# Optimization experiments

Measured on AMD Instinct MI355X. Metric: run time of the kernel, lower is better.

## Reference

```python
import jax, jax.numpy as jnp
from jax import lax
import numpy as np
import math

B, L, UNITS, DM, P = 2048, 2, 16, 512, 16
CH = UNITS // P            # 1  (attention 'head' dim c)
D = DM // P                # 32
C_ATT = CH * D             # 32 channels in patch space
C_FFN = 4 * C_ATT          # 128
HALF = P // 2              # 8 (post-stride-2 patch size)
EPS = 1e-5


def _to_patches(x):
    # 'b (c p1) (d p2) -> b (c d) p1 p2'
    b = x.shape[0]
    x = x.reshape(b, CH, P, D, P).transpose(0, 1, 3, 2, 4)
    return x.reshape(b, CH * D, P, P)


def _from_patches(x):
    # 'b (c d) p1 p2 -> b (c p1) (d p2)'
    b = x.shape[0]
    x = x.reshape(b, CH, D, P, P).transpose(0, 1, 3, 2, 4)
    return x.reshape(b, CH * P, D * P)


def _layernorm(x, g, b):
    m = jnp.mean(x, -1, keepdims=True)
    v = jnp.mean((x - m) ** 2, -1, keepdims=True)
    return (x - m) * lax.rsqrt(v + EPS) * g + b


def _dw_block(x, dw_w, dw_b, bn_g, bn_b, bn_m, bn_v, pw_w, pw_b, stride):
    # depthwise 3x3 conv -> BatchNorm (eval) -> 1x1 pointwise conv
    C = x.shape[1]
    y = lax.conv_general_dilated(
        x, dw_w[:, None], (stride, stride), [(1, 1), (1, 1)],
        dimension_numbers=('NCHW', 'OIHW', 'NCHW'), feature_group_count=C)
    if dw_b is not None:
        y = y + dw_b[None, :, None, None]
    scale = (bn_g * lax.rsqrt(bn_v + EPS))[None, :, None, None]
    y = (y - bn_m[None, :, None, None]) * scale + bn_b[None, :, None, None]
    y = jnp.einsum('bchw,oc->bohw', y, pw_w)
    if pw_b is not None:
        y = y + pw_b[None, :, None, None]
    return y


def _encoder(x, ln1_g, ln1_b, ln2_g, ln2_b, qkv_dw, qkv_bng, qkv_bnb, qkv_bnm,
             qkv_bnv, qkv_pw, position, c1d_w, c1d_b, lin_w, lin_b,
             f1_w, f1_b, fdw_w, fdw_b, f_bng, f_bnb, f_bnm, f_bnv,
             fpw_w, fpw_b, f2_w, f2_b):
    b = x.shape[0]
    for l in range(L):
        # ---- attention sublayer (pre-norm) ----
        x1 = _layernorm(x, ln1_g[l], ln1_b[l])
        xp = _to_patches(x1)                              # (B, 32, 16, 16)
        qkv = [_dw_block(xp, qkv_dw[l, i], None,
                         qkv_bng[l, i], qkv_bnb[l, i], qkv_bnm[l, i], qkv_bnv[l, i],
                         qkv_pw[l, i], None, 2)           # (B, 32, 8, 8)
               .reshape(b, CH, D, HALF * HALF)            # 'b (c d) p1 p2 -> b c d (p1 p2)'
               for i in range(3)]
        q, k, v = qkv
        scores = jnp.einsum('bcde,bcfe->bcdf', q, k) / math.sqrt(HALF * HALF)
        scores = scores + position[l][None]               # (B, 1, 32, 32)
        p_attn = jax.nn.softmax(scores, axis=-1)
        o = jnp.einsum('bcdf,bcfe->bcde', p_attn, v)      # (B, 1, 32, 64)
        # 'b c d (p1 p2) -> b (c p1) (d p2)' with p1 = P//2
        o = o.reshape(b, CH, D, HALF, HALF).transpose(0, 1, 3, 2, 4)
        o = o.reshape(b, CH * HALF, D * HALF)             # (B, 8, 256)
        o = jnp.einsum('bcd,oc->bod', o, c1d_w[l]) + c1d_b[l][None, :, None]
        o = jnp.einsum('bcd,od->bco', o, lin_w[l]) + lin_b[l]  # (B, 16, 512)
        x = x + o
        # ---- conv-FFN sublayer ----
        x2 = _layernorm(x, ln2_g[l], ln2_b[l])
        y = _to_patches(x2)                               # (B, 32, 16, 16)
        y = jnp.einsum('bchw,oc->bohw', y, f1_w[l]) + f1_b[l][None, :, None, None]
        y = jax.nn.relu(y)                                # (B, 128, 16, 16)
        y = _dw_block(y, fdw_w[l], fdw_b[l], f_bng[l], f_bnb[l], f_bnm[l],
                      f_bnv[l], fpw_w[l], fpw_b[l], 1)
        y = jax.nn.relu(y)
        y = jnp.einsum('bchw,oc->bohw', y, f2_w[l]) + f2_b[l][None, :, None, None]
        x = x + _from_patches(y)
    return x


def setup_inputs():
    key = jax.random.key(0)
    ks = iter(jax.random.split(key, 16))
    nrm = lambda shape, s=0.05: jax.random.normal(next(ks), shape, jnp.float32) * s
    return dict(
        x=jax.random.normal(next(ks), (B, UNITS, DM), jnp.float32),
        ln1_g=jnp.ones((L, DM)), ln1_b=jnp.zeros((L, DM)),
        ln2_g=jnp.ones((L, DM)), ln2_b=jnp.zeros((L, DM)),
        qkv_dw=nrm((L, 3, C_ATT, 3, 3)),
        qkv_bng=jnp.ones((L, 3, C_ATT)), qkv_bnb=jnp.zeros((L, 3, C_ATT)),
        qkv_bnm=jnp.zeros((L, 3, C_ATT)), qkv_bnv=jnp.ones((L, 3, C_ATT)),
        qkv_pw=nrm((L, 3, C_ATT, C_ATT)),
        position=nrm((L, CH, D, D), 1.0),
        c1d_w=nrm((L, UNITS, UNITS // 2)), c1d_b=jnp.zeros((L, UNITS)),
        lin_w=nrm((L, DM, DM // 2)), lin_b=jnp.zeros((L, DM)),
        f1_w=nrm((L, C_FFN, C_ATT)), f1_b=jnp.zeros((L, C_FFN)),
        fdw_w=nrm((L, C_FFN, 3, 3)), fdw_b=jnp.zeros((L, C_FFN)),
        f_bng=jnp.ones((L, C_FFN)), f_bnb=jnp.zeros((L, C_FFN)),
        f_bnm=jnp.zeros((L, C_FFN)), f_bnv=jnp.ones((L, C_FFN)),
        fpw_w=nrm((L, C_FFN, C_FFN)), fpw_b=jnp.zeros((L, C_FFN)),
        f2_w=nrm((L, C_ATT, C_FFN)), f2_b=jnp.zeros((L, C_ATT)),
    )


def reference(x, ln1_g, ln1_b, ln2_g, ln2_b, qkv_dw, qkv_bng, qkv_bnb, qkv_bnm,
              qkv_bnv, qkv_pw, position, c1d_w, c1d_b, lin_w, lin_b,
              f1_w, f1_b, fdw_w, fdw_b, f_bng, f_bnb, f_bnm, f_bnv,
              fpw_w, fpw_b, f2_w, f2_b):
    return _encoder(x, ln1_g, ln1_b, ln2_g, ln2_b, qkv_dw, qkv_bng, qkv_bnb,
                    qkv_bnm, qkv_bnv, qkv_pw, position, c1d_w, c1d_b, lin_w,
                    lin_b, f1_w, f1_b, fdw_w, fdw_b, f_bng, f_bnb, f_bnm,
                    f_bnv, fpw_w, fpw_b, f2_w, f2_b)
```

## Files before the change

kernel.cpp:

```cpp
#include <hip/hip_runtime.h>
#include <hip/hip_bf16.h>

#define B_ 2048
#define EPSF 1e-5f

typedef __attribute__((ext_vector_type(8))) short short8v;
typedef __attribute__((ext_vector_type(4))) short short4v;
typedef __attribute__((ext_vector_type(4))) float f32x4;

__device__ __forceinline__ short f2bf_s(float f) {
  union { float f; unsigned u; } v; v.f = f;
  unsigned r = v.u + 0x7fffu + ((v.u >> 16) & 1u);
  return (short)(r >> 16);
}
__device__ __forceinline__ float bf2f(short s) {
  return __uint_as_float(((unsigned)(unsigned short)s) << 16);
}

__global__ __launch_bounds__(256) void k_prep(
    const float* __restrict__ f1_w, const float* __restrict__ fpw_w,
    const float* __restrict__ f2_w, const float* __restrict__ qkv_pw,
    const float* __restrict__ lin_w, const float* __restrict__ fdw_w,
    const float* __restrict__ fdw_b, const float* __restrict__ f_bng,
    const float* __restrict__ f_bnb, const float* __restrict__ f_bnm,
    const float* __restrict__ f_bnv, short* __restrict__ qkvA,
    short* __restrict__ linb, short* __restrict__ f1wb,
    short* __restrict__ img, float* __restrict__ convW,
    float* __restrict__ convB) {
  int i = blockIdx.x * 256 + threadIdx.x;
  if (i < 7680) {
    int l = i / 3840, r = i % 3840;
    int io = r / 40, c = r % 40;
    qkvA[i] = (c < 32) ? f2bf_s(qkv_pw[l * 3072 + io * 32 + c]) : (short)0;
  }
  if (i < 262144) linb[i] = f2bf_s(lin_w[i]);
  if (i < 10240) {
    int l = i / 5120, r = i % 5120, o = r / 40, kk = r % 40;
    f1wb[i] = (kk < 32) ? f2bf_s(f1_w[l * 4096 + o * 32 + kk]) : (short)0;
  }
  if (i < 48640) {
    int l = i / 24320, r = i % 24320;
    short val;
    if (r < 19456) {
      int o = r / 152, kk = r % 152;
      val = (kk < 128) ? f2bf_s(fpw_w[l * 16384 + o * 128 + kk]) : (short)0;
    } else {
      int r2 = r - 19456;
      int d = r2 / 152, kk = r2 % 152;
      val = (kk < 128) ? f2bf_s(f2_w[l * 4096 + d * 128 + kk]) : (short)0;
    }
    img[i] = val;
  }
  if (i < 256) {
    int l = i >> 7, c = i & 127;
    float scale = f_bng[l * 128 + c] * rsqrtf(f_bnv[l * 128 + c] + EPSF);
#pragma unroll
    for (int k = 0; k < 9; k++)
      convW[l * 1152 + k * 128 + c] = fdw_w[(l * 128 + c) * 9 + k] * scale;
    convB[l * 128 + c] =
        (fdw_b[l * 128 + c] - f_bnm[l * 128 + c]) * scale + f_bnb[l * 128 + c];
  }
}

__device__ __forceinline__ void ln_to_patches(const float* __restrict__ xb,
                                              const float* __restrict__ g,
                                              const float* __restrict__ beta,
                                              float (*p)[257], int tid) {
  int lane = tid & 63, wave = tid >> 6;
  for (int r = wave; r < 16; r += 4) {
    float vals[8];
    float s = 0.f, ss = 0.f;
#pragma unroll
    for (int j = 0; j < 8; j++) {
      float t = xb[r * 512 + lane + j * 64];
      vals[j] = t; s += t; ss += t * t;
    }
#pragma unroll
    for (int o = 32; o; o >>= 1) { s += __shfl_xor(s, o); ss += __shfl_xor(ss, o); }
    float m = s * (1.f / 512.f);
    float inv = rsqrtf(ss * (1.f / 512.f) - m * m + EPSF);
#pragma unroll
    for (int j = 0; j < 8; j++) {
      int col = lane + j * 64;
      p[col >> 4][r * 16 + (col & 15)] = (vals[j] - m) * inv * g[col] + beta[col];
    }
  }
}

__global__ __launch_bounds__(256) void k_att(
    const float* __restrict__ x, const float* __restrict__ g,
    const float* __restrict__ beta, const float* __restrict__ dw,
    const float* __restrict__ bng, const float* __restrict__ bnb,
    const float* __restrict__ bnm, const float* __restrict__ bnv,
    const short* __restrict__ qkvA, const float* __restrict__ posn,
    const float* __restrict__ c1w, const float* __restrict__ c1b,
    const short* __restrict__ linb, const float* __restrict__ lin_b,
    float* __restrict__ xg) {
  __shared__ __align__(16) char smem[62592];
  float (*p)[257] = (float(*)[257])smem;
  float* sc  = (float*)(smem + 0);
  short* pa  = (short*)(smem + 4224);
  short* ore = (short*)(smem + 6784);
  short* xc1 = (short*)(smem + 11008);
  short* t3s = (short*)(smem + 32896);
  short* qe  = (short*)(smem + 48256);
  short* ke  = (short*)(smem + 52864);
  short* vt  = (short*)(smem + 57472);

  int b = blockIdx.x, tid = threadIdx.x;
  int lane = tid & 63, wid = tid >> 6;
  int row = lane & 15, kg = lane >> 4;
  const float* xb = x + (size_t)b * 8192;

  ln_to_patches(xb, g, beta, p, tid);
  __syncthreads();

  {
    int c = tid & 31, oy = tid >> 5;
    float r0[16], r1[16], r2[16];
    int iy0 = 2 * oy - 1;
#pragma unroll
    for (int i = 0; i < 16; i++) {
      r0[i] = (iy0 >= 0) ? p[c][iy0 * 16 + i] : 0.f;
      r1[i] = p[c][(2 * oy) * 16 + i];
      r2[i] = p[c][(2 * oy + 1) * 16 + i];
    }
    for (int iw = 0; iw < 3; iw++) {
      const float* w9 = dw + iw * 288 + c * 9;
      float w00 = w9[0], w01 = w9[1], w02 = w9[2];
      float w10 = w9[3], w11 = w9[4], w12 = w9[5];
      float w20 = w9[6], w21 = w9[7], w22 = w9[8];
      float scale = bng[iw * 32 + c] * rsqrtf(bnv[iw * 32 + c] + EPSF);
      float shift = bnb[iw * 32 + c] - bnm[iw * 32 + c] * scale;
#pragma unroll
      for (int ox = 0; ox < 8; ox++) {
        int ix = 2 * ox;
        float acc = w01 * r0[ix] + w11 * r1[ix] + w21 * r2[ix]
                  + w02 * r0[ix + 1] + w12 * r1[ix + 1] + w22 * r2[ix + 1];
        if (ix > 0) acc += w00 * r0[ix - 1] + w10 * r1[ix - 1] + w20 * r2[ix - 1];
        t3s[(iw * 64 + oy * 8 + ox) * 40 + c] = f2bf_s(acc * scale + shift);
      }
    }
  }
  __syncthreads();

  {
    int mi = wid & 1, nbase = (wid >> 1) * 2;
    for (int iw = 0; iw < 3; iw++) {
      short8v a = *(const short8v*)&qkvA[(iw * 32 + mi * 16 + row) * 40 + kg * 8];
      short8v b0 = *(const short8v*)&t3s[(iw * 64 + (nbase + 0) * 16 + row) * 40 + kg * 8];
      short8v b1 = *(const short8v*)&t3s[(iw * 64 + (nbase + 1) * 16 + row) * 40 + kg * 8];
      f32x4 z = {};
      f32x4 acc0 = __builtin_amdgcn_mfma_f32_16x16x32_bf16(a, b0, z, 0, 0, 0);
      f32x4 acc1 = __builtin_amdgcn_mfma_f32_16x16x32_bf16(a, b1, z, 0, 0, 0);
      if (iw < 2) {
        short* tgt = (iw == 0) ? qe : ke;
#pragma unroll
        for (int r = 0; r < 4; r++) {
          int d = mi * 16 + kg * 4 + r;
          tgt[d * 72 + (nbase + 0) * 16 + row] = f2bf_s(acc0[r]);
          tgt[d * 72 + (nbase + 1) * 16 + row] = f2bf_s(acc1[r]);
        }
      } else {
        int e0 = (nbase + 0) * 16 + row, e1 = (nbase + 1) * 16 + row;
        int fb = mi * 16 + kg * 4;
        short4v v0, v1;
        v0.x = f2bf_s(acc0[0]); v0.y = f2bf_s(acc0[1]);
        v0.z = f2bf_s(acc0[2]); v0.w = f2bf_s(acc0[3]);
        v1.x = f2bf_s(acc1[0]); v1.y = f2bf_s(acc1[1]);
        v1.z = f2bf_s(acc1[2]); v1.w = f2bf_s(acc1[3]);
        *(short4v*)&vt[e0 * 40 + fb] = v0;
        *(short4v*)&vt[e1 * 40 + fb] = v1;
      }
    }
  }
  __syncthreads();

  {
    int mi = wid & 1, ni = wid >> 1;
    f32x4 acc = {};
#pragma unroll
    for (int kk = 0; kk < 2; kk++) {
      short8v a = *(const short8v*)&qe[(mi * 16 + row) * 72 + kk * 32 + kg * 8];
      short8v bb = *(const short8v*)&ke[(ni * 16 + row) * 72 + kk * 32 + kg * 8];
      acc = __builtin_amdgcn_mfma_f32_16x16x32_bf16(a, bb, acc, 0, 0, 0);
    }
#pragma unroll
    for (int r = 0; r < 4; r++) {
      int d = mi * 16 + kg * 4 + r, f = ni * 16 + row;
      sc[d * 33 + f] = acc[r] * 0.125f + posn[d * 32 + f];
    }
  }
  __syncthreads();

  {
    int srow = tid >> 3, sg = tid & 7;
    float v0 = sc[srow * 33 + sg * 4 + 0];
    float v1 = sc[srow * 33 + sg * 4 + 1];
    float v2 = sc[srow * 33 + sg * 4 + 2];
    float v3 = sc[srow * 33 + sg * 4 + 3];
    float mx = fmaxf(fmaxf(v0, v1), fmaxf(v2, v3));
    mx = fmaxf(mx, __shfl_xor(mx, 1));
    mx = fmaxf(mx, __shfl_xor(mx, 2));
    mx = fmaxf(mx, __shfl_xor(mx, 4));
    float e0 = __expf(v0 - mx), e1 = __expf(v1 - mx);
    float e2 = __expf(v2 - mx), e3 = __expf(v3 - mx);
    float s = e0 + e1 + e2 + e3;
    s += __shfl_xor(s, 1); s += __shfl_xor(s, 2); s += __shfl_xor(s, 4);
    float inv = 1.f / s;
    short4v pk;
    pk.x = f2bf_s(e0 * inv); pk.y = f2bf_s(e1 * inv);
    pk.z = f2bf_s(e2 * inv); pk.w = f2bf_s(e3 * inv);
    *(short4v*)&pa[srow * 40 + sg * 4] = pk;
  }
  __syncthreads();

  {
    int mi = wid & 1, nbase = (wid >> 1) * 2;
    short8v a = *(const short8v*)&pa[(mi * 16 + row) * 40 + kg * 8];
#pragma unroll
    for (int t = 0; t < 2; t++) {
      int e = (nbase + t) * 16 + row;
      short8v bb = *(const short8v*)&vt[e * 40 + kg * 8];
      f32x4 z = {};
      f32x4 acc = __builtin_amdgcn_mfma_f32_16x16x32_bf16(a, bb, z, 0, 0, 0);
#pragma unroll
      for (int r = 0; r < 4; r++) {
        int d = mi * 16 + kg * 4 + r;
        ore[(e >> 3) * 264 + d * 8 + (e & 7)] = f2bf_s(acc[r]);
      }
    }
  }
  __syncthreads();

  {
    int n = tid;
#pragma unroll
    for (int u = 0; u < 16; u++) {
      float acc = c1b[u];
#pragma unroll
      for (int c = 0; c < 8; c++)
        acc += c1w[u * 8 + c] * bf2f(ore[c * 264 + n]);
      xc1[u * 264 + n] = f2bf_s(acc);
    }
  }
  __syncthreads();

  {
    short8v a8[8];
#pragma unroll
    for (int kk = 0; kk < 8; kk++)
      a8[kk] = *(const short8v*)&xc1[row * 264 + kk * 32 + kg * 8];
    float* xo = xg + (size_t)b * 8192;
    for (int t = 0; t < 8; t++) {
      int nt = wid * 8 + t;
      const short* bb_base = linb + (nt * 16 + row) * 256 + kg * 8;
      f32x4 acc = {};
#pragma unroll
      for (int kk = 0; kk < 8; kk++) {
        short8v bb = *(const short8v*)(bb_base + kk * 32);
        acc = __builtin_amdgcn_mfma_f32_16x16x32_bf16(a8[kk], bb, acc, 0, 0, 0);
      }
      int m = nt * 16 + row;
      float lb = lin_b[m];
#pragma unroll
      for (int r = 0; r < 4; r++) {
        int u = kg * 4 + r;
        xo[u * 512 + m] += acc[r] + lb;
      }
    }
  }
}

__global__ __launch_bounds__(1024, 4) void k_ffn4(
    const float* __restrict__ x, const float* __restrict__ g,
    const float* __restrict__ beta, const short* __restrict__ f1wg,
    const float* __restrict__ f1b, const float* __restrict__ convW,
    const float* __restrict__ convB, const short* __restrict__ img,
    const float* __restrict__ pwbias, const float* __restrict__ f2b,
    float* __restrict__ xg) {
  __shared__ __align__(16) char smem[149504];
  short* p_lds = (short*)smem;
  short* f1w_lds = (short*)(smem + 20480);
  short* sT = (short*)smem;
  short* sY = (short*)(smem + 77824);
  short* pw_lds = (short*)(smem + 77824);
  short* f2w_lds = (short*)(smem + 77824 + 38912);
  float* f2out = (float*)(smem + 77824);

  int b = blockIdx.x, tid = threadIdx.x;
  int lane = tid & 63, wid = tid >> 6;
  int row = lane & 15, kg = lane >> 4;
  const float* xb = x + (size_t)b * 8192;
  float* xo = xg + (size_t)b * 8192;

  const uint4* imgu = (const uint4*)img;
  uint4 pf0 = imgu[tid], pf1 = imgu[tid + 1024];
  uint4 pf2 = {};
  if (tid < 992) pf2 = imgu[tid + 2048];

  if (tid < 640) ((uint4*)f1w_lds)[tid] = ((const uint4*)f1wg)[tid];

  {
    int r = wid;
    float vals[8];
    float s = 0.f, ss = 0.f;
#pragma unroll
    for (int j = 0; j < 8; j++) {
      float t = xb[r * 512 + lane + j * 64];
      vals[j] = t; s += t; ss += t * t;
    }
#pragma unroll
    for (int o = 32; o; o >>= 1) { s += __shfl_xor(s, o); ss += __shfl_xor(ss, o); }
    float m = s * (1.f / 512.f);
    float inv = rsqrtf(ss * (1.f / 512.f) - m * m + EPSF);
#pragma unroll
    for (int j = 0; j < 8; j++) {
      int col = lane + j * 64;
      float nv = (vals[j] - m) * inv * g[col] + beta[col];
      p_lds[(r * 16 + (col & 15)) * 40 + (col >> 4)] = f2bf_s(nv);
    }
  }
  __syncthreads();

  {
    int o0 = (wid & 3) * 32, pos0 = (wid >> 2) * 64;
    short8v a0 = *(const short8v*)&f1w_lds[(o0 + row) * 40 + kg * 8];
    short8v a1 = *(const short8v*)&f1w_lds[(o0 + 16 + row) * 40 + kg * 8];
#pragma unroll
    for (int ni = 0; ni < 4; ni++) {
      short8v bb = *(const short8v*)&p_lds[(pos0 + ni * 16 + row) * 40 + kg * 8];
      f32x4 z = {};
      f32x4 c0 = __builtin_amdgcn_mfma_f32_16x16x32_bf16(a0, bb, z, 0, 0, 0);
      f32x4 c1 = __builtin_amdgcn_mfma_f32_16x16x32_bf16(a1, bb, z, 0, 0, 0);
      int pos = pos0 + ni * 16 + row;
#pragma unroll
      for (int r2 = 0; r2 < 4; r2++) {
        int c = o0 + kg * 4 + r2;
        sY[c * 280 + pos] = f2bf_s(fmaxf(c0[r2] + f1b[c], 0.f));
        sY[(c + 16) * 280 + pos] = f2bf_s(fmaxf(c1[r2] + f1b[c + 16], 0.f));
      }
    }
  }
  __syncthreads();

  {
    int c = tid & 127, strip = tid >> 7;
    float w_[9];
#pragma unroll
    for (int k = 0; k < 9; k++) w_[k] = convW[k * 128 + c];
    float cb = convB[c];
#pragma unroll
    for (int j = 0; j < 2; j++) {
      int h = strip * 2 + j;
      float acc[16];
#pragma unroll
      for (int w = 0; w < 16; w++) acc[w] = cb;
#pragma unroll
      for (int rr = 0; rr < 3; rr++) {
        int rg = h - 1 + rr;
        if (rg < 0 || rg > 15) continue;
        short8v s0 = *(const short8v*)&sY[c * 280 + rg * 16];
        short8v s1 = *(const short8v*)&sY[c * 280 + rg * 16 + 8];
        float f[18];
        f[0] = 0.f; f[17] = 0.f;
#pragma unroll
        for (int i = 0; i < 8; i++) { f[1 + i] = bf2f(s0[i]); f[9 + i] = bf2f(s1[i]); }
        float w0 = w_[rr * 3], w1 = w_[rr * 3 + 1], w2 = w_[rr * 3 + 2];
#pragma unroll
        for (int w = 0; w < 16; w++)
          acc[w] += w0 * f[w] + w1 * f[w + 1] + w2 * f[w + 2];
      }
#pragma unroll
      for (int w = 0; w < 16; w++)
        sT[(h * 16 + w) * 152 + c] = f2bf_s(acc[w]);
    }
  }
  __syncthreads();

  {
    uint4* wdst = (uint4*)pw_lds;
    wdst[tid] = pf0; wdst[tid + 1024] = pf1;
    if (tid < 992) wdst[tid + 2048] = pf2;
  }
  __syncthreads();

  int o0 = (wid & 3) * 32, pos0 = (wid >> 2) * 64;
  f32x4 facc[2][4] = {};
#pragma unroll
  for (int kk = 0; kk < 4; kk++) {
    int k0 = kk * 32 + kg * 8;
    short8v a0 = *(const short8v*)&pw_lds[(o0 + row) * 152 + k0];
    short8v a1 = *(const short8v*)&pw_lds[(o0 + 16 + row) * 152 + k0];
    short8v bb[4];
#pragma unroll
    for (int ni = 0; ni < 4; ni++)
      bb[ni] = *(const short8v*)&sT[(pos0 + ni * 16 + row) * 152 + k0];
#pragma unroll
    for (int ni = 0; ni < 4; ni++) {
      facc[0][ni] = __builtin_amdgcn_mfma_f32_16x16x32_bf16(a0, bb[ni], facc[0][ni], 0, 0, 0);
      facc[1][ni] = __builtin_amdgcn_mfma_f32_16x16x32_bf16(a1, bb[ni], facc[1][ni], 0, 0, 0);
    }
  }
  __syncthreads();

#pragma unroll
  for (int mi = 0; mi < 2; mi++) {
    int ob = o0 + mi * 16 + kg * 4;
    float pb0 = pwbias[ob], pb1 = pwbias[ob + 1];
    float pb2 = pwbias[ob + 2], pb3 = pwbias[ob + 3];
#pragma unroll
    for (int ni = 0; ni < 4; ni++) {
      int pos = pos0 + ni * 16 + row;
      short4v pk;
      pk.x = f2bf_s(fmaxf(facc[mi][ni][0] + pb0, 0.f));
      pk.y = f2bf_s(fmaxf(facc[mi][ni][1] + pb1, 0.f));
      pk.z = f2bf_s(fmaxf(facc[mi][ni][2] + pb2, 0.f));
      pk.w = f2bf_s(fmaxf(facc[mi][ni][3] + pb3, 0.f));
      *(short4v*)&sT[pos * 152 + ob] = pk;
    }
  }
  __syncthreads();

  {
    f32x4 acc2[2] = {};
    int pos = wid * 16 + row;
#pragma unroll
    for (int kk = 0; kk < 4; kk++) {
      int k0 = kk * 32 + kg * 8;
      short8v a0 = *(const short8v*)&f2w_lds[row * 152 + k0];
      short8v a1 = *(const short8v*)&f2w_lds[(16 + row) * 152 + k0];
      short8v bb = *(const short8v*)&sT[pos * 152 + k0];
      acc2[0] = __builtin_amdgcn_mfma_f32_16x16x32_bf16(a0, bb, acc2[0], 0, 0, 0);
      acc2[1] = __builtin_amdgcn_mfma_f32_16x16x32_bf16(a1, bb, acc2[1], 0, 0, 0);
    }
#pragma unroll
    for (int mi = 0; mi < 2; mi++)
#pragma unroll
      for (int r2 = 0; r2 < 4; r2++) {
        int d = mi * 16 + kg * 4 + r2;
        f2out[d * 257 + pos] = acc2[mi][r2];
      }
  }
  __syncthreads();

#pragma unroll
  for (int j = 0; j < 8; j++) {
    int idx = tid + j * 1024;
    int dm = idx & 511;
    int d = dm >> 4, p2 = dm & 15;
    int p1 = idx >> 9;
    xo[idx] += f2out[d * 257 + p1 * 16 + p2] + f2b[d];
  }
}

extern "C" void kernel_launch(void* const* d_in, const int* in_sizes, int n_in,
                              void* d_out, int out_size, void* d_ws, size_t ws_size,
                              hipStream_t stream) {
  const float* x_in   = (const float*)d_in[0];
  const float* ln1_g  = (const float*)d_in[1];
  const float* ln1_b  = (const float*)d_in[2];
  const float* ln2_g  = (const float*)d_in[3];
  const float* ln2_b  = (const float*)d_in[4];
  const float* qkv_dw = (const float*)d_in[5];
  const float* qkv_bng = (const float*)d_in[6];
  const float* qkv_bnb = (const float*)d_in[7];
  const float* qkv_bnm = (const float*)d_in[8];
  const float* qkv_bnv = (const float*)d_in[9];
  const float* qkv_pw = (const float*)d_in[10];
  const float* position = (const float*)d_in[11];
  const float* c1d_w  = (const float*)d_in[12];
  const float* c1d_b  = (const float*)d_in[13];
  const float* lin_w  = (const float*)d_in[14];
  const float* lin_b  = (const float*)d_in[15];
  const float* f1_w   = (const float*)d_in[16];
  const float* f1_b   = (const float*)d_in[17];
  const float* fdw_w  = (const float*)d_in[18];
  const float* fdw_b  = (const float*)d_in[19];
  const float* f_bng  = (const float*)d_in[20];
  const float* f_bnb  = (const float*)d_in[21];
  const float* f_bnm  = (const float*)d_in[22];
  const float* f_bnv  = (const float*)d_in[23];
  const float* fpw_w  = (const float*)d_in[24];
  const float* fpw_b  = (const float*)d_in[25];
  const float* f2_w   = (const float*)d_in[26];
  const float* f2_b   = (const float*)d_in[27];

  float* xbuf = (float*)d_out;
  short* qkvA = (short*)d_ws;
  short* linb = qkvA + 7680;
  short* f1wb = linb + 262144;
  short* img  = f1wb + 10240;
  float* convW = (float*)(img + 48640);
  float* convB = convW + 2304;

  hipMemcpyAsync(xbuf, x_in, (size_t)B_ * 8192 * sizeof(float),
                 hipMemcpyDeviceToDevice, stream);
  k_prep<<<1024, 256, 0, stream>>>(f1_w, fpw_w, f2_w, qkv_pw, lin_w,
      fdw_w, fdw_b, f_bng, f_bnb, f_bnm, f_bnv,
      qkvA, linb, f1wb, img, convW, convB);
  for (int l = 0; l < 2; l++) {
    k_att<<<B_, 256, 0, stream>>>(xbuf, ln1_g + l * 512, ln1_b + l * 512,
        qkv_dw + l * 864, qkv_bng + l * 96, qkv_bnb + l * 96,
        qkv_bnm + l * 96, qkv_bnv + l * 96, qkvA + l * 3840,
        position + l * 1024, c1d_w + l * 128, c1d_b + l * 16,
        linb + l * 131072, lin_b + l * 512, xbuf);
    k_ffn4<<<B_, 1024, 0, stream>>>(xbuf, ln2_g + l * 512, ln2_b + l * 512,
        f1wb + l * 5120, f1_b + l * 128, convW + l * 1152, convB + l * 128,
        img + l * 24320, fpw_b + l * 128, f2_b + l * 32, xbuf);
  }
}
```

Baseline: 423.2 us.

## Drop input memcpy, write residuals directly, double attention block threads

The first attention kernel now reads the original input and writes its result to the output buffer, so the upfront device-to-device copy is gone. Both kernels preload their residual values into registers and write x+delta directly instead of doing a read-modify-write. The FFN kernel also skips its LDS staging pass and the extra barrier at the end. The attention kernel moves from 256 to 512 threads per block, splitting the conv, MFMA, conv1d and linear stages across more waves, though some stages leave half the threads idle. The risks are more register pressure from the held residuals and uncoalesced direct global stores.

Measured after the change: 400.1 us. 1.06x faster.

```diff
diff --git a/kernel.cpp b/kernel.cpp
--- a/kernel.cpp
+++ b/kernel.cpp
@@ -62,40 +62,15 @@
   }
 }
 
-__device__ __forceinline__ void ln_to_patches(const float* __restrict__ xb,
-                                              const float* __restrict__ g,
-                                              const float* __restrict__ beta,
-                                              float (*p)[257], int tid) {
-  int lane = tid & 63, wave = tid >> 6;
-  for (int r = wave; r < 16; r += 4) {
-    float vals[8];
-    float s = 0.f, ss = 0.f;
-#pragma unroll
-    for (int j = 0; j < 8; j++) {
-      float t = xb[r * 512 + lane + j * 64];
-      vals[j] = t; s += t; ss += t * t;
-    }
-#pragma unroll
-    for (int o = 32; o; o >>= 1) { s += __shfl_xor(s, o); ss += __shfl_xor(ss, o); }
-    float m = s * (1.f / 512.f);
-    float inv = rsqrtf(ss * (1.f / 512.f) - m * m + EPSF);
-#pragma unroll
-    for (int j = 0; j < 8; j++) {
-      int col = lane + j * 64;
-      p[col >> 4][r * 16 + (col & 15)] = (vals[j] - m) * inv * g[col] + beta[col];
-    }
-  }
-}
-
-__global__ __launch_bounds__(256) void k_att(
-    const float* __restrict__ x, const float* __restrict__ g,
+__global__ __launch_bounds__(512) void k_att(
+    const float* __restrict__ xin, const float* __restrict__ g,
     const float* __restrict__ beta, const float* __restrict__ dw,
     const float* __restrict__ bng, const float* __restrict__ bnb,
     const float* __restrict__ bnm, const float* __restrict__ bnv,
     const short* __restrict__ qkvA, const float* __restrict__ posn,
     const float* __restrict__ c1w, const float* __restrict__ c1b,
     const short* __restrict__ linb, const float* __restrict__ lin_b,
-    float* __restrict__ xg) {
+    float* __restrict__ xout) {
   __shared__ __align__(16) char smem[62592];
   float (*p)[257] = (float(*)[257])smem;
   float* sc  = (float*)(smem + 0);
@@ -110,20 +85,48 @@
   int b = blockIdx.x, tid = threadIdx.x;
   int lane = tid & 63, wid = tid >> 6;
   int row = lane & 15, kg = lane >> 4;
-  const float* xb = x + (size_t)b * 8192;
-
-  ln_to_patches(xb, g, beta, p, tid);
-  __syncthreads();
-
-  {
-    int c = tid & 31, oy = tid >> 5;
-    float r0[16], r1[16], r2[16];
+  const float* xb = xin + (size_t)b * 8192;
+  float* xo = xout + (size_t)b * 8192;
+
+  float xr[4][4];
+#pragma unroll
+  for (int t = 0; t < 4; t++)
+#pragma unroll
+    for (int r = 0; r < 4; r++)
+      xr[t][r] = xb[(kg * 4 + r) * 512 + (wid * 4 + t) * 16 + row];
+
+  for (int r = wid; r < 16; r += 8) {
+    float vals[8];
+    float s = 0.f, ss = 0.f;
+#pragma unroll
+    for (int j = 0; j < 8; j++) {
+      float t = xb[r * 512 + lane + j * 64];
+      vals[j] = t; s += t; ss += t * t;
+    }
+#pragma unroll
+    for (int o = 32; o; o >>= 1) { s += __shfl_xor(s, o); ss += __shfl_xor(ss, o); }
+    float m = s * (1.f / 512.f);
+    float inv = rsqrtf(ss * (1.f / 512.f) - m * m + EPSF);
+#pragma unroll
+    for (int j = 0; j < 8; j++) {
+      int col = lane + j * 64;
+      p[col >> 4][r * 16 + (col & 15)] = (vals[j] - m) * inv * g[col] + beta[col];
+    }
+  }
+  __syncthreads();
+
+  {
+    int c = tid & 31, oy = (tid >> 5) & 7, oxh = tid >> 8;
+    int base = oxh * 8 - 1;
+    float ra[9], rb[9], rc[9];
     int iy0 = 2 * oy - 1;
 #pragma unroll
-    for (int i = 0; i < 16; i++) {
-      r0[i] = (iy0 >= 0) ? p[c][iy0 * 16 + i] : 0.f;
-      r1[i] = p[c][(2 * oy) * 16 + i];
-      r2[i] = p[c][(2 * oy + 1) * 16 + i];
+    for (int k = 0; k < 9; k++) {
+      int ic = base + k;
+      bool cv = (ic >= 0);
+      ra[k] = (cv && iy0 >= 0) ? p[c][iy0 * 16 + ic] : 0.f;
+      rb[k] = cv ? p[c][(2 * oy) * 16 + ic] : 0.f;
+      rc[k] = cv ? p[c][(2 * oy + 1) * 16 + ic] : 0.f;
     }
     for (int iw = 0; iw < 3; iw++) {
       const float* w9 = dw + iw * 288 + c * 9;
@@ -133,11 +136,11 @@
       float scale = bng[iw * 32 + c] * rsqrtf(bnv[iw * 32 + c] + EPSF);
       float shift = bnb[iw * 32 + c] - bnm[iw * 32 + c] * scale;
 #pragma unroll
-      for (int ox = 0; ox < 8; ox++) {
-        int ix = 2 * ox;
-        float acc = w01 * r0[ix] + w11 * r1[ix] + w21 * r2[ix]
-                  + w02 * r0[ix + 1] + w12 * r1[ix + 1] + w22 * r2[ix + 1];
-        if (ix > 0) acc += w00 * r0[ix - 1] + w10 * r1[ix - 1] + w20 * r2[ix - 1];
+      for (int j = 0; j < 4; j++) {
+        int ox = oxh * 4 + j;
+        float acc = w00 * ra[2 * j] + w01 * ra[2 * j + 1] + w02 * ra[2 * j + 2]
+                  + w10 * rb[2 * j] + w11 * rb[2 * j + 1] + w12 * rb[2 * j + 2]
+                  + w20 * rc[2 * j] + w21 * rc[2 * j + 1] + w22 * rc[2 * j + 2];
         t3s[(iw * 64 + oy * 8 + ox) * 40 + c] = f2bf_s(acc * scale + shift);
       }
     }
@@ -145,39 +148,33 @@
   __syncthreads();
 
   {
-    int mi = wid & 1, nbase = (wid >> 1) * 2;
+    int mi = wid & 1, ni = wid >> 1;
     for (int iw = 0; iw < 3; iw++) {
       short8v a = *(const short8v*)&qkvA[(iw * 32 + mi * 16 + row) * 40 + kg * 8];
-      short8v b0 = *(const short8v*)&t3s[(iw * 64 + (nbase + 0) * 16 + row) * 40 + kg * 8];
-      short8v b1 = *(const short8v*)&t3s[(iw * 64 + (nbase + 1) * 16 + row) * 40 + kg * 8];
+      short8v bb = *(const short8v*)&t3s[(iw * 64 + ni * 16 + row) * 40 + kg * 8];
       f32x4 z = {};
-      f32x4 acc0 = __builtin_amdgcn_mfma_f32_16x16x32_bf16(a, b0, z, 0, 0, 0);
-      f32x4 acc1 = __builtin_amdgcn_mfma_f32_16x16x32_bf16(a, b1, z, 0, 0, 0);
+      f32x4 acc = __builtin_amdgcn_mfma_f32_16x16x32_bf16(a, bb, z, 0, 0, 0);
       if (iw < 2) {
         short* tgt = (iw == 0) ? qe : ke;
 #pragma unroll
         for (int r = 0; r < 4; r++) {
           int d = mi * 16 + kg * 4 + r;
-          tgt[d * 72 + (nbase + 0) * 16 + row] = f2bf_s(acc0[r]);
-          tgt[d * 72 + (nbase + 1) * 16 + row] = f2bf_s(acc1[r]);
+          tgt[d * 72 + ni * 16 + row] = f2bf_s(acc[r]);
         }
       } else {
-        int e0 = (nbase + 0) * 16 + row, e1 = (nbase + 1) * 16 + row;
+        int e = ni * 16 + row;
         int fb = mi * 16 + kg * 4;
-        short4v v0, v1;
-        v0.x = f2bf_s(acc0[0]); v0.y = f2bf_s(acc0[1]);
-        v0.z = f2bf_s(acc0[2]); v0.w = f2bf_s(acc0[3]);
-        v1.x = f2bf_s(acc1[0]); v1.y = f2bf_s(acc1[1]);
-        v1.z = f2bf_s(acc1[2]); v1.w = f2bf_s(acc1[3]);
-        *(short4v*)&vt[e0 * 40 + fb] = v0;
-        *(short4v*)&vt[e1 * 40 + fb] = v1;
-      }
-    }
-  }
-  __syncthreads();
-
-  {
-    int mi = wid & 1, ni = wid >> 1;
+        short4v v0;
+        v0.x = f2bf_s(acc[0]); v0.y = f2bf_s(acc[1]);
+        v0.z = f2bf_s(acc[2]); v0.w = f2bf_s(acc[3]);
+        *(short4v*)&vt[e * 40 + fb] = v0;
+      }
+    }
+  }
+  __syncthreads();
+
+  if (wid < 4) {
+    int mi = wid & 1, ni = (wid >> 1) & 1;
     f32x4 acc = {};
 #pragma unroll
     for (int kk = 0; kk < 2; kk++) {
@@ -193,7 +190,7 @@
   }
   __syncthreads();
 
-  {
+  if (tid < 256) {
     int srow = tid >> 3, sg = tid & 7;
     float v0 = sc[srow * 33 + sg * 4 + 0];
     float v1 = sc[srow * 33 + sg * 4 + 1];
@@ -216,31 +213,31 @@
   __syncthreads();
 
   {
-    int mi = wid & 1, nbase = (wid >> 1) * 2;
+    int mi = wid & 1, et = wid >> 1;
     short8v a = *(const short8v*)&pa[(mi * 16 + row) * 40 + kg * 8];
-#pragma unroll
-    for (int t = 0; t < 2; t++) {
-      int e = (nbase + t) * 16 + row;
-      short8v bb = *(const short8v*)&vt[e * 40 + kg * 8];
-      f32x4 z = {};
-      f32x4 acc = __builtin_amdgcn_mfma_f32_16x16x32_bf16(a, bb, z, 0, 0, 0);
-#pragma unroll
-      for (int r = 0; r < 4; r++) {
-        int d = mi * 16 + kg * 4 + r;
-        ore[(e >> 3) * 264 + d * 8 + (e & 7)] = f2bf_s(acc[r]);
-      }
-    }
-  }
-  __syncthreads();
-
-  {
-    int n = tid;
-#pragma unroll
-    for (int u = 0; u < 16; u++) {
+    int e = et * 16 + row;
+    short8v bb = *(const short8v*)&vt[e * 40 + kg * 8];
+    f32x4 z = {};
+    f32x4 acc = __builtin_amdgcn_mfma_f32_16x16x32_bf16(a, bb, z, 0, 0, 0);
+#pragma unroll
+    for (int r = 0; r < 4; r++) {
+      int d = mi * 16 + kg * 4 + r;
+      ore[(e >> 3) * 264 + d * 8 + (e & 7)] = f2bf_s(acc[r]);
+    }
+  }
+  __syncthreads();
+
+  {
+    int n = tid & 255, uh = tid >> 8;
+    float o8[8];
+#pragma unroll
+    for (int c = 0; c < 8; c++) o8[c] = bf2f(ore[c * 264 + n]);
+#pragma unroll
+    for (int uu = 0; uu < 8; uu++) {
+      int u = uh * 8 + uu;
       float acc = c1b[u];
 #pragma unroll
-      for (int c = 0; c < 8; c++)
-        acc += c1w[u * 8 + c] * bf2f(ore[c * 264 + n]);
+      for (int c = 0; c < 8; c++) acc += c1w[u * 8 + c] * o8[c];
       xc1[u * 264 + n] = f2bf_s(acc);
     }
   }
@@ -251,9 +248,9 @@
 #pragma unroll
     for (int kk = 0; kk < 8; kk++)
       a8[kk] = *(const short8v*)&xc1[row * 264 + kk * 32 + kg * 8];
-    float* xo = xg + (size_t)b * 8192;
-    for (int t = 0; t < 8; t++) {
-      int nt = wid * 8 + t;
+#pragma unroll
+    for (int t = 0; t < 4; t++) {
+      int nt = wid * 4 + t;
       const short* bb_base = linb + (nt * 16 + row) * 256 + kg * 8;
       f32x4 acc = {};
 #pragma unroll
@@ -266,7 +263,7 @@
 #pragma unroll
       for (int r = 0; r < 4; r++) {
         int u = kg * 4 + r;
-        xo[u * 512 + m] += acc[r] + lb;
+        xo[u * 512 + m] = xr[t][r] + acc[r] + lb;
       }
     }
   }
@@ -286,7 +283,6 @@
   short* sY = (short*)(smem + 77824);
   short* pw_lds = (short*)(smem + 77824);
   short* f2w_lds = (short*)(smem + 77824 + 38912);
-  float* f2out = (float*)(smem + 77824);
 
   int b = blockIdx.x, tid = threadIdx.x;
   int lane = tid & 63, wid = tid >> 6;
@@ -298,6 +294,13 @@
   uint4 pf0 = imgu[tid], pf1 = imgu[tid + 1024];
   uint4 pf2 = {};
   if (tid < 992) pf2 = imgu[tid + 2048];
+
+  float xr[2][4];
+#pragma unroll
+  for (int mi = 0; mi < 2; mi++)
+#pragma unroll
+    for (int r2 = 0; r2 < 4; r2++)
+      xr[mi][r2] = xo[wid * 512 + mi * 256 + kg * 64 + r2 * 16 + row];
 
   if (tid < 640) ((uint4*)f1w_lds)[tid] = ((const uint4*)f1wg)[tid];
 
@@ -439,18 +442,9 @@
 #pragma unroll
       for (int r2 = 0; r2 < 4; r2++) {
         int d = mi * 16 + kg * 4 + r2;
-        f2out[d * 257 + pos] = acc2[mi][r2];
-      }
-  }
-  __syncthreads();
-
-#pragma unroll
-  for (int j = 0; j < 8; j++) {
-    int idx = tid + j * 1024;
-    int dm = idx & 511;
-    int d = dm >> 4, p2 = dm & 15;
-    int p1 = idx >> 9;
-    xo[idx] += f2out[d * 257 + p1 * 16 + p2] + f2b[d];
+        xo[wid * 512 + mi * 256 + kg * 64 + r2 * 16 + row] =
+            xr[mi][r2] + acc2[mi][r2] + f2b[d];
+      }
   }
 }
 
@@ -494,13 +488,12 @@
   float* convW = (float*)(img + 48640);
   float* convB = convW + 2304;
 
-  hipMemcpyAsync(xbuf, x_in, (size_t)B_ * 8192 * sizeof(float),
-                 hipMemcpyDeviceToDevice, stream);
   k_prep<<<1024, 256, 0, stream>>>(f1_w, fpw_w, f2_w, qkv_pw, lin_w,
       fdw_w, fdw_b, f_bng, f_bnb, f_bnm, f_bnv,
       qkvA, linb, f1wb, img, convW, convB);
   for (int l = 0; l < 2; l++) {
-    k_att<<<B_, 256, 0, stream>>>(xbuf, ln1_g + l * 512, ln1_b + l * 512,
+    const float* xin = (l == 0) ? x_in : xbuf;
+    k_att<<<B_, 512, 0, stream>>>(xin, ln1_g + l * 512, ln1_b + l * 512,
         qkv_dw + l * 864, qkv_bng + l * 96, qkv_bnb + l * 96,
         qkv_bnm + l * 96, qkv_bnv + l * 96, qkvA + l * 3840,
         position + l * 1024, c1d_w + l * 128, c1d_b + l * 16,
```
